# Kernel tuning notes

Measured on AMD Instinct MI355X. Metric: run time of the kernel, lower is better.

Reference implementation:

```python
import jax, jax.numpy as jnp
import numpy as np

N_NODES = 50000
N_EDGES = 800000
N_IN = 96
N_HID = 96
N_CLS = 16
P_DROP = 0.5


def setup_inputs() -> dict:
    key = jax.random.key(0)
    ks = jax.random.split(key, 10)
    return {
        "features": jax.random.normal(ks[0], (N_NODES, N_IN), dtype=jnp.float32),
        "edge_weight": jax.random.uniform(ks[1], (N_EDGES,), dtype=jnp.float32),
        "src": jax.random.randint(ks[2], (N_EDGES,), 0, N_NODES),
        "dst": jax.random.randint(ks[3], (N_EDGES,), 0, N_NODES),
        "W0": jax.random.normal(ks[4], (N_IN, N_HID), dtype=jnp.float32) / np.sqrt(N_IN).astype(np.float32),
        "b0": jnp.zeros((N_HID,), dtype=jnp.float32),
        "W1": jax.random.normal(ks[5], (N_HID, N_HID), dtype=jnp.float32) / np.sqrt(N_HID).astype(np.float32),
        "b1": jnp.zeros((N_HID,), dtype=jnp.float32),
        "W2": jax.random.normal(ks[6], (N_HID, N_CLS), dtype=jnp.float32) / np.sqrt(N_HID).astype(np.float32),
        "b2": jnp.zeros((N_CLS,), dtype=jnp.float32),
    }


def reference(features, edge_weight, src, dst, W0, b0, W1, b1, W2, b2):
    N = features.shape[0]
    # Unweighted node degrees (DGL GraphConv norm='both'), clamped to >= 1.
    ones_e = jnp.ones_like(edge_weight)
    out_deg = jnp.clip(jax.ops.segment_sum(ones_e, src, num_segments=N), 1.0)
    in_deg = jnp.clip(jax.ops.segment_sum(ones_e, dst, num_segments=N), 1.0)
    inv_sqrt_out = out_deg ** -0.5  # [N]
    inv_sqrt_in = in_deg ** -0.5    # [N]

    def graph_conv(h, W, b, act):
        h = h * inv_sqrt_out[:, None]
        m = h[src] * edge_weight[:, None]                   # [E, d] gather + edge scale
        agg = jax.ops.segment_sum(m, dst, num_segments=N)   # [N, d] scatter-add
        out = (agg * inv_sqrt_in[:, None]) @ W + b          # D_in^-1/2, then linear + bias
        return act(out) if act is not None else out

    layers = [(W0, b0, jax.nn.relu), (W1, b1, jax.nn.relu), (W2, b2, None)]
    dkey = jax.random.key(42)
    h = features
    for i, (W, b, act) in enumerate(layers):
        keep = jax.random.bernoulli(jax.random.fold_in(dkey, i), 1.0 - P_DROP, h.shape)
        h = jnp.where(keep, h / (1.0 - P_DROP), 0.0)        # dropout p=0.5
        h = graph_conv(h, W, b, act)
    return jax.nn.log_softmax(h, axis=1)
```

## Files before the change

kernel.cpp:

```cpp
#include <hip/hip_runtime.h>
#include <hip/hip_fp16.h>
#include <stdint.h>

#define NNODES 50000
#define NEDGES 800000
#define NHID 96
#define NCLS 16

#define NC 100
#define NR 4
#define EPB (NEDGES / NC)
#define RNODES (NNODES / NR)
#define RWORDS8 (RNODES / 4)
#define NWORDS8 (NNODES / 4)
#define SCANB ((NWORDS8 + 255) / 256)
#define HISTBLKS (NC * NR)
#define FEPT 4
#define FILLB2 ((NEDGES / FEPT + 255) / 256)
#define NDROP4 ((NNODES * NHID / 4 + 255) / 256)

__host__ __device__ inline void tf2x32(uint32_t k0, uint32_t k1, uint32_t x0, uint32_t x1,
                                       uint32_t& o0, uint32_t& o1) {
  uint32_t k2 = k0 ^ k1 ^ 0x1BD11BDAu;
#define TFROT(v, r) (((v) << (r)) | ((v) >> (32 - (r))))
#define TFR(r) { x0 += x1; x1 = TFROT(x1, r); x1 ^= x0; }
  x0 += k0; x1 += k1;
  TFR(13) TFR(15) TFR(26) TFR(6)
  x0 += k1; x1 += k2 + 1u;
  TFR(17) TFR(29) TFR(16) TFR(24)
  x0 += k2; x1 += k0 + 2u;
  TFR(13) TFR(15) TFR(26) TFR(6)
  x0 += k0; x1 += k1 + 3u;
  TFR(17) TFR(29) TFR(16) TFR(24)
  x0 += k1; x1 += k2 + 4u;
  TFR(13) TFR(15) TFR(26) TFR(6)
  x0 += k2; x1 += k0 + 5u;
  o0 = x0; o1 = x1;
#undef TFR
#undef TFROT
}

__device__ inline bool keep_bit(uint32_t k0, uint32_t k1, uint32_t j) {
  uint32_t o0, o1;
  tf2x32(k0, k1, 0u, j, o0, o1);
  return (((o0 ^ o1) >> 31) == 0u);
}

__global__ __launch_bounds__(256) void hist_drop_kernel(
    const int* __restrict__ src, const int* __restrict__ dst,
    uint32_t* __restrict__ slabD, uint32_t* __restrict__ slabS,
    uint8_t* __restrict__ rank8, uint32_t* __restrict__ flags,
    const float* __restrict__ h, float* __restrict__ X,
    uint32_t k0, uint32_t k1) {
  __shared__ uint32_t HD[RWORDS8];
  __shared__ uint32_t HS[RWORDS8];
  const int tid = threadIdx.x, b = blockIdx.x;
  if (b >= HISTBLKS) {
    int j = ((b - HISTBLKS) * 256 + tid) * 4;
    if (j < NNODES * NHID) {
      float4 hv = *(const float4*)(h + j);
      float4 o;
      o.x = keep_bit(k0, k1, (uint32_t)(j + 0)) ? hv.x * 2.0f : 0.0f;
      o.y = keep_bit(k0, k1, (uint32_t)(j + 1)) ? hv.y * 2.0f : 0.0f;
      o.z = keep_bit(k0, k1, (uint32_t)(j + 2)) ? hv.z * 2.0f : 0.0f;
      o.w = keep_bit(k0, k1, (uint32_t)(j + 3)) ? hv.w * 2.0f : 0.0f;
      *(float4*)(X + j) = o;
    }
    return;
  }
  if (b == 0 && tid < SCANB) flags[tid] = 0;
  const int c = b / NR, r = b - c * NR;
  const int e0 = c * EPB, e1 = e0 + EPB;
  const int nbase = r * RNODES;
  for (int w = tid; w < RWORDS8; w += 256) { HD[w] = 0; HS[w] = 0; }
  __syncthreads();
  int e = e0 + tid;
  for (; e + 768 < e1; e += 1024) {
    int d0 = dst[e] - nbase,       d1 = dst[e + 256] - nbase;
    int d2 = dst[e + 512] - nbase, d3 = dst[e + 768] - nbase;
    int s0 = src[e] - nbase,       s1 = src[e + 256] - nbase;
    int s2 = src[e + 512] - nbase, s3 = src[e + 768] - nbase;
    if ((unsigned)d0 < (unsigned)RNODES) {
      int sh = (d0 & 3) * 8;
      uint32_t old = atomicAdd(&HD[d0 >> 2], 1u << sh);
      rank8[e] = (uint8_t)((old >> sh) & 0xFFu);
    }
    if ((unsigned)d1 < (unsigned)RNODES) {
      int sh = (d1 & 3) * 8;
      uint32_t old = atomicAdd(&HD[d1 >> 2], 1u << sh);
      rank8[e + 256] = (uint8_t)((old >> sh) & 0xFFu);
    }
    if ((unsigned)d2 < (unsigned)RNODES) {
      int sh = (d2 & 3) * 8;
      uint32_t old = atomicAdd(&HD[d2 >> 2], 1u << sh);
      rank8[e + 512] = (uint8_t)((old >> sh) & 0xFFu);
    }
    if ((unsigned)d3 < (unsigned)RNODES) {
      int sh = (d3 & 3) * 8;
      uint32_t old = atomicAdd(&HD[d3 >> 2], 1u << sh);
      rank8[e + 768] = (uint8_t)((old >> sh) & 0xFFu);
    }
    if ((unsigned)s0 < (unsigned)RNODES) atomicAdd(&HS[s0 >> 2], 1u << ((s0 & 3) * 8));
    if ((unsigned)s1 < (unsigned)RNODES) atomicAdd(&HS[s1 >> 2], 1u << ((s1 & 3) * 8));
    if ((unsigned)s2 < (unsigned)RNODES) atomicAdd(&HS[s2 >> 2], 1u << ((s2 & 3) * 8));
    if ((unsigned)s3 < (unsigned)RNODES) atomicAdd(&HS[s3 >> 2], 1u << ((s3 & 3) * 8));
  }
  for (; e < e1; e += 256) {
    int d = dst[e] - nbase;
    if ((unsigned)d < (unsigned)RNODES) {
      int sh = (d & 3) * 8;
      uint32_t old = atomicAdd(&HD[d >> 2], 1u << sh);
      rank8[e] = (uint8_t)((old >> sh) & 0xFFu);
    }
    int s = src[e] - nbase;
    if ((unsigned)s < (unsigned)RNODES) atomicAdd(&HS[s >> 2], 1u << ((s & 3) * 8));
  }
  __syncthreads();
  uint32_t* dpD = slabD + (size_t)b * RWORDS8;
  uint32_t* dpS = slabS + (size_t)b * RWORDS8;
  for (int w = tid; w < RWORDS8; w += 256) { dpD[w] = HD[w]; dpS[w] = HS[w]; }
}

__global__ __launch_bounds__(256) void reduce_scan_kernel(
    const uint32_t* __restrict__ slabD, const uint32_t* __restrict__ slabS,
    float* __restrict__ inv_o, float* __restrict__ inv_i,
    uint32_t* __restrict__ rel8, int* __restrict__ row_ptr,
    uint32_t* __restrict__ flags) {
  __shared__ int lds[256];
  __shared__ int base_s;
  const int tid = threadIdx.x, b = blockIdx.x;
  const int gw = b * 256 + tid;
  uint32_t runD = 0, runS = 0;
  int n0 = 0;
  if (gw < NWORDS8) {
    int r = gw / RWORDS8, lw = gw - r * RWORDS8;
    n0 = r * RNODES + 4 * lw;
#pragma unroll 4
    for (int c = 0; c < NC; ++c) {
      rel8[(size_t)c * NWORDS8 + gw] = runD;
      runD += slabD[(size_t)(c * NR + r) * RWORDS8 + lw];
      runS += slabS[(size_t)(c * NR + r) * RWORDS8 + lw];
    }
  }
  const int d0 = runD & 0xFF, d1 = (runD >> 8) & 0xFF,
            d2 = (runD >> 16) & 0xFF, d3 = runD >> 24;
  const int tsum = d0 + d1 + d2 + d3;
  lds[tid] = tsum;
  __syncthreads();
  for (int off = 1; off < 256; off <<= 1) {
    int t = (tid >= off) ? lds[tid - off] : 0;
    __syncthreads();
    lds[tid] += t;
    __syncthreads();
  }
  const int incl = lds[tid];
  if (tid == 255) atomicExch(&flags[b], 0x80000000u | (uint32_t)lds[255]);
  if (tid < 64) {
    uint32_t part = 0;
    if (tid < b) {
      uint32_t v;
      do { v = atomicAdd(&flags[tid], 0u); } while (!(v & 0x80000000u));
      part = v & 0x7FFFFFFFu;
    }
#pragma unroll
    for (int off = 32; off > 0; off >>= 1)
      part += __shfl_down((unsigned)part, off, 64);
    if (tid == 0) base_s = (int)part;
  }
  __syncthreads();
  const int base = base_s;
  if (gw < NWORDS8) {
    int excl = base + incl - tsum;
    *(int4*)(row_ptr + n0) = make_int4(excl, excl + d0, excl + d0 + d1, excl + d0 + d1 + d2);
    *(float4*)(inv_i + n0) = make_float4(
        rsqrtf(fmaxf((float)d0, 1.0f)), rsqrtf(fmaxf((float)d1, 1.0f)),
        rsqrtf(fmaxf((float)d2, 1.0f)), rsqrtf(fmaxf((float)d3, 1.0f)));
    int o0 = runS & 0xFF, o1 = (runS >> 8) & 0xFF, o2 = (runS >> 16) & 0xFF, o3 = runS >> 24;
    *(float4*)(inv_o + n0) = make_float4(
        rsqrtf(fmaxf((float)o0, 1.0f)), rsqrtf(fmaxf((float)o1, 1.0f)),
        rsqrtf(fmaxf((float)o2, 1.0f)), rsqrtf(fmaxf((float)o3, 1.0f)));
    if (gw == NWORDS8 - 1) row_ptr[NNODES] = NEDGES;
  }
}

__global__ __launch_bounds__(256) void fill_kernel(
    const int* __restrict__ src, const int* __restrict__ dst, const float* __restrict__ ew,
    const uint8_t* __restrict__ rank8, const uint32_t* __restrict__ rel8,
    const int* __restrict__ row_ptr, const float* __restrict__ inv_o,
    uint32_t* __restrict__ csr) {
  int t = blockIdx.x * 256 + threadIdx.x;
  int e = t * 4;
  if (e >= NEDGES) return;
  int4 d4 = *(const int4*)(dst + e);
  int4 s4 = *(const int4*)(src + e);
  float4 w4 = *(const float4*)(ew + e);
  uint32_t r4 = *(const uint32_t*)(rank8 + e);
  const uint32_t* rel = rel8 + (size_t)(e / EPB) * NWORDS8;
#pragma unroll
  for (int k = 0; k < 4; ++k) {
    int d = (&d4.x)[k];
    int s = (&s4.x)[k];
    float w = (&w4.x)[k] * inv_o[s];
    int rk = (int)((r4 >> (k * 8)) & 0xFFu);
    int sh = (d & 3) * 8;
    int rel_v = (int)((rel[d >> 2] >> sh) & 0xFFu);
    int pos = row_ptr[d] + rel_v + rk;
    uint32_t v = ((uint32_t)s << 16) | (uint32_t)__half_as_ushort(__float2half_rn(w));
    if ((unsigned)pos < (unsigned)NEDGES) csr[pos] = v;
  }
}

__global__ __launch_bounds__(256) void gemm96_kernel(
    const float* __restrict__ X, const float* __restrict__ W, __half* __restrict__ Yh) {
  __shared__ float Wl[96 * 96];
  const int tid = threadIdx.x;
  {
    const float4* Wg = (const float4*)W;
    float4* Ws = (float4*)Wl;
#pragma unroll
    for (int i = 0; i < 9; ++i)
      Ws[tid + i * 256] = Wg[tid + i * 256];
  }
  __syncthreads();

  const int cg = tid & 7;
  const int rq = tid >> 3;
  const int row0 = blockIdx.x * 128 + rq * 4;
  const int c0 = cg * 12;

  float acc[4][12];
#pragma unroll
  for (int r = 0; r < 4; ++r)
#pragma unroll
    for (int c = 0; c < 12; ++c) acc[r][c] = 0.f;

  const float* xr[4];
#pragma unroll
  for (int r = 0; r < 4; ++r) {
    int rr = row0 + r; if (rr > NNODES - 1) rr = NNODES - 1;
    xr[r] = X + (size_t)rr * 96;
  }

  for (int k = 0; k < 96; k += 4) {
    float4 x4[4];
#pragma unroll
    for (int r = 0; r < 4; ++r) x4[r] = *(const float4*)(xr[r] + k);
#pragma unroll
    for (int kk = 0; kk < 4; ++kk) {
      const float4* wp = (const float4*)(Wl + (k + kk) * 96 + c0);
      float4 w0 = wp[0], w1 = wp[1], w2 = wp[2];
      float xv[4] = { (&x4[0].x)[kk], (&x4[1].x)[kk], (&x4[2].x)[kk], (&x4[3].x)[kk] };
#pragma unroll
      for (int r = 0; r < 4; ++r) {
        acc[r][0]  += xv[r] * w0.x; acc[r][1]  += xv[r] * w0.y;
        acc[r][2]  += xv[r] * w0.z; acc[r][3]  += xv[r] * w0.w;
        acc[r][4]  += xv[r] * w1.x; acc[r][5]  += xv[r] * w1.y;
        acc[r][6]  += xv[r] * w1.z; acc[r][7]  += xv[r] * w1.w;
        acc[r][8]  += xv[r] * w2.x; acc[r][9]  += xv[r] * w2.y;
        acc[r][10] += xv[r] * w2.z; acc[r][11] += xv[r] * w2.w;
      }
    }
  }

#pragma unroll
  for (int r = 0; r < 4; ++r) {
    int rr = row0 + r;
    if (rr < NNODES) {
      __half2* hp = (__half2*)(Yh + (size_t)rr * 96 + c0);
#pragma unroll
      for (int c = 0; c < 6; ++c)
        hp[c] = __floats2half2_rn(acc[r][2 * c], acc[r][2 * c + 1]);
    }
  }
}

__global__ __launch_bounds__(256) void gemm16_kernel(
    const float* __restrict__ X, const float* __restrict__ W, __half* __restrict__ Y2h) {
  __shared__ float Wl[96 * 16];
  const int tid = threadIdx.x;
  {
    const float4* Wg = (const float4*)W;
    float4* Ws = (float4*)Wl;
    for (int i = tid; i < 384; i += 256) Ws[i] = Wg[i];
  }
  __syncthreads();

  const int row0 = blockIdx.x * 512 + tid * 2;
  const float* xr[2];
#pragma unroll
  for (int r = 0; r < 2; ++r) {
    int rr = row0 + r; if (rr > NNODES - 1) rr = NNODES - 1;
    xr[r] = X + (size_t)rr * 96;
  }

  float acc[2][16];
#pragma unroll
  for (int r = 0; r < 2; ++r)
#pragma unroll
    for (int c = 0; c < 16; ++c) acc[r][c] = 0.f;

  for (int k = 0; k < 96; k += 4) {
    float4 x4[2];
#pragma unroll
    for (int r = 0; r < 2; ++r) x4[r] = *(const float4*)(xr[r] + k);
#pragma unroll
    for (int kk = 0; kk < 4; ++kk) {
      const float4* wp = (const float4*)(Wl + (k + kk) * 16);
      float4 w0 = wp[0], w1 = wp[1], w2 = wp[2], w3 = wp[3];
#pragma unroll
      for (int r = 0; r < 2; ++r) {
        float xv = (&x4[r].x)[kk];
        acc[r][0]  += xv * w0.x; acc[r][1]  += xv * w0.y;
        acc[r][2]  += xv * w0.z; acc[r][3]  += xv * w0.w;
        acc[r][4]  += xv * w1.x; acc[r][5]  += xv * w1.y;
        acc[r][6]  += xv * w1.z; acc[r][7]  += xv * w1.w;
        acc[r][8]  += xv * w2.x; acc[r][9]  += xv * w2.y;
        acc[r][10] += xv * w2.z; acc[r][11] += xv * w2.w;
        acc[r][12] += xv * w3.x; acc[r][13] += xv * w3.y;
        acc[r][14] += xv * w3.z; acc[r][15] += xv * w3.w;
      }
    }
  }

#pragma unroll
  for (int r = 0; r < 2; ++r) {
    int rr = row0 + r;
    if (rr < NNODES) {
      __half2* hp = (__half2*)(Y2h + (size_t)rr * 16);
#pragma unroll
      for (int c = 0; c < 8; ++c)
        hp[c] = __floats2half2_rn(acc[r][2 * c], acc[r][2 * c + 1]);
    }
  }
}

#define ACC8(u0, wt) { \
  float2 g0 = __half22float2(*(__half2*)&u0.x); \
  float2 g1 = __half22float2(*(__half2*)&u0.y); \
  float2 g2 = __half22float2(*(__half2*)&u0.z); \
  float2 g3 = __half22float2(*(__half2*)&u0.w); \
  acc[0] += g0.x * wt; acc[1] += g0.y * wt; \
  acc[2] += g1.x * wt; acc[3] += g1.y * wt; \
  acc[4] += g2.x * wt; acc[5] += g2.y * wt; \
  acc[6] += g3.x * wt; acc[7] += g3.y * wt; }

__global__ __launch_bounds__(256) void gather96_drop_kernel(
    const __half* __restrict__ Yh, const uint32_t* __restrict__ csr,
    const int* __restrict__ row_ptr, const float* __restrict__ inv_in,
    const float* __restrict__ bias,
    float* __restrict__ Xn, uint32_t k0, uint32_t k1) {
  int tid = blockIdx.x * 256 + threadIdx.x;
  int n = tid / 12;
  int q = tid - n * 12;
  if (n >= NNODES) return;
  int beg = row_ptr[n], end = row_ptr[n + 1];
  float acc[8];
#pragma unroll
  for (int i = 0; i < 8; ++i) acc[i] = 0.f;

  int p = beg;
  for (; p + 8 <= end; p += 8) {
    uint32_t pw[8];
#pragma unroll
    for (int i = 0; i < 8; ++i) pw[i] = csr[p + i];
    float wv[8];
    uint4 u[8];
#pragma unroll
    for (int i = 0; i < 8; ++i) {
      int s = (int)(pw[i] >> 16); if (s >= NNODES) s = 0;
      wv[i] = __half2float(__ushort_as_half((unsigned short)(pw[i] & 0xFFFFu)));
      u[i] = *(const uint4*)(Yh + (size_t)s * 96 + q * 8);
    }
#pragma unroll
    for (int i = 0; i < 8; ++i) { ACC8(u[i], wv[i]) }
  }
  for (; p + 2 <= end; p += 2) {
    uint32_t pa = csr[p], pb = csr[p + 1];
    int s0 = pa >> 16, s1 = pb >> 16;
    if (s0 >= NNODES) s0 = 0;
    if (s1 >= NNODES) s1 = 0;
    float w0 = __half2float(__ushort_as_half((unsigned short)(pa & 0xFFFFu)));
    float w1 = __half2float(__ushort_as_half((unsigned short)(pb & 0xFFFFu)));
    uint4 a0 = *(const uint4*)(Yh + (size_t)s0 * 96 + q * 8);
    uint4 b0 = *(const uint4*)(Yh + (size_t)s1 * 96 + q * 8);
    ACC8(a0, w0)
    ACC8(b0, w1)
  }
  if (p < end) {
    uint32_t pa = csr[p];
    int s0 = pa >> 16;
    if (s0 >= NNODES) s0 = 0;
    float w0 = __half2float(__ushort_as_half((unsigned short)(pa & 0xFFFFu)));
    uint4 a0 = *(const uint4*)(Yh + (size_t)s0 * 96 + q * 8);
    ACC8(a0, w0)
  }

  float iv = inv_in[n];
  const float* bp = bias + q * 8;
  float o[8];
#pragma unroll
  for (int i = 0; i < 8; ++i)
    o[i] = fmaxf(acc[i] * iv + bp[i], 0.f) * 2.0f;
  uint32_t jb = (uint32_t)(n * 96 + q * 8);
#pragma unroll
  for (int i = 0; i < 8; ++i)
    o[i] = keep_bit(k0, k1, jb + i) ? o[i] : 0.f;
  float* xp = Xn + (size_t)n * 96 + q * 8;
  *(float4*)(xp + 0) = make_float4(o[0], o[1], o[2], o[3]);
  *(float4*)(xp + 4) = make_float4(o[4], o[5], o[6], o[7]);
}

__global__ __launch_bounds__(256) void gather16_lsm_kernel(
    const __half* __restrict__ Y2h, const uint32_t* __restrict__ csr,
    const int* __restrict__ row_ptr, const float* __restrict__ inv_in,
    const float* __restrict__ b2, float* __restrict__ out) {
  int t = blockIdx.x * 256 + threadIdx.x;
  int n = t >> 1;
  int q = t & 1;
  if (n >= NNODES) return;
  int beg = row_ptr[n], end = row_ptr[n + 1];
  float acc[8];
#pragma unroll
  for (int i = 0; i < 8; ++i) acc[i] = 0.f;

  int p = beg;
  for (; p + 4 <= end; p += 4) {
    uint32_t pa = csr[p], pb = csr[p + 1], pc = csr[p + 2], pd = csr[p + 3];
    int sa = pa >> 16, sb = pb >> 16, sc_ = pc >> 16, sd = pd >> 16;
    if (sa >= NNODES) sa = 0;
    if (sb >= NNODES) sb = 0;
    if (sc_ >= NNODES) sc_ = 0;
    if (sd >= NNODES) sd = 0;
    float wa = __half2float(__ushort_as_half((unsigned short)(pa & 0xFFFFu)));
    float wb = __half2float(__ushort_as_half((unsigned short)(pb & 0xFFFFu)));
    float wc = __half2float(__ushort_as_half((unsigned short)(pc & 0xFFFFu)));
    float wd = __half2float(__ushort_as_half((unsigned short)(pd & 0xFFFFu)));
    uint4 a0 = *(const uint4*)(Y2h + (size_t)sa * 16 + q * 8);
    uint4 b0 = *(const uint4*)(Y2h + (size_t)sb * 16 + q * 8);
    uint4 c0 = *(const uint4*)(Y2h + (size_t)sc_ * 16 + q * 8);
    uint4 d0 = *(const uint4*)(Y2h + (size_t)sd * 16 + q * 8);
    ACC8(a0, wa) ACC8(b0, wb) ACC8(c0, wc) ACC8(d0, wd)
  }
  for (; p + 2 <= end; p += 2) {
    uint32_t pa = csr[p], pb = csr[p + 1];
    int sa = pa >> 16, sb = pb >> 16;
    if (sa >= NNODES) sa = 0;
    if (sb >= NNODES) sb = 0;
    float wa = __half2float(__ushort_as_half((unsigned short)(pa & 0xFFFFu)));
    float wb = __half2float(__ushort_as_half((unsigned short)(pb & 0xFFFFu)));
    uint4 a0 = *(const uint4*)(Y2h + (size_t)sa * 16 + q * 8);
    uint4 b0 = *(const uint4*)(Y2h + (size_t)sb * 16 + q * 8);
    ACC8(a0, wa) ACC8(b0, wb)
  }
  if (p < end) {
    uint32_t pa = csr[p];
    int sa = pa >> 16;
    if (sa >= NNODES) sa = 0;
    float wa = __half2float(__ushort_as_half((unsigned short)(pa & 0xFFFFu)));
    uint4 a0 = *(const uint4*)(Y2h + (size_t)sa * 16 + q * 8);
    ACC8(a0, wa)
  }

  float iv = inv_in[n];
  float v[8];
#pragma unroll
  for (int i = 0; i < 8; ++i) v[i] = acc[i] * iv + b2[q * 8 + i];
  float m = v[0];
#pragma unroll
  for (int i = 1; i < 8; i++) m = fmaxf(m, v[i]);
  m = fmaxf(m, __shfl_xor(m, 1));
  float s = 0.f;
#pragma unroll
  for (int i = 0; i < 8; i++) s += expf(v[i] - m);
  s += __shfl_xor(s, 1);
  float ls = logf(s);
  float* orow = out + (size_t)n * 16 + q * 8;
  *(float4*)(orow + 0) = make_float4(v[0] - m - ls, v[1] - m - ls, v[2] - m - ls, v[3] - m - ls);
  *(float4*)(orow + 4) = make_float4(v[4] - m - ls, v[5] - m - ls, v[6] - m - ls, v[7] - m - ls);
}

extern "C" void kernel_launch(void* const* d_in, const int* in_sizes, int n_in,
                              void* d_out, int out_size, void* d_ws, size_t ws_size,
                              hipStream_t stream) {
  const float* feat = (const float*)d_in[0];
  const float* ew   = (const float*)d_in[1];
  const int*   src  = (const int*)d_in[2];
  const int*   dst  = (const int*)d_in[3];
  const float* W0   = (const float*)d_in[4];
  const float* b0   = (const float*)d_in[5];
  const float* W1   = (const float*)d_in[6];
  const float* b1   = (const float*)d_in[7];
  const float* W2   = (const float*)d_in[8];
  const float* b2   = (const float*)d_in[9];
  float* out = (float*)d_out;

  char* base = (char*)d_ws;
  size_t off = 0;
  auto take = [&](size_t nbytes) {
    void* q = base + off;
    off += (nbytes + 255) & ~(size_t)255;
    return q;
  };
  uint32_t* flags   = (uint32_t*)take((size_t)SCANB * 4);
  int*      row_ptr = (int*)take((size_t)(NNODES + 1) * 4);
  float*    inv_o   = (float*)take((size_t)NNODES * 4);
  float*    inv_i   = (float*)take((size_t)NNODES * 4);
  uint32_t* slabD   = (uint32_t*)take((size_t)NC * NR * RWORDS8 * 4);
  uint32_t* slabS   = (uint32_t*)take((size_t)NC * NR * RWORDS8 * 4);
  uint32_t* rel8    = (uint32_t*)take((size_t)NC * NWORDS8 * 4);
  uint8_t*  rank8   = (uint8_t*)take((size_t)NEDGES);
  uint32_t* csr     = (uint32_t*)take((size_t)NEDGES * 4);
  float*    X       = (float*)take((size_t)NNODES * NHID * 4);
  __half*   Yh      = (__half*)take((size_t)NNODES * NHID * 2);
  __half*   Y2h     = (__half*)take((size_t)NNODES * NCLS * 2);
  (void)ws_size; (void)in_sizes; (void)n_in; (void)out_size;

  uint32_t k[3][2];
  for (uint32_t i = 0; i < 3; i++) tf2x32(0u, 42u, 0u, i, k[i][0], k[i][1]);

  hist_drop_kernel<<<HISTBLKS + NDROP4, 256, 0, stream>>>(
      src, dst, slabD, slabS, rank8, flags, feat, X, k[0][0], k[0][1]);
  reduce_scan_kernel<<<SCANB, 256, 0, stream>>>(slabD, slabS, inv_o, inv_i, rel8, row_ptr, flags);
  fill_kernel<<<FILLB2, 256, 0, stream>>>(src, dst, ew, rank8, rel8, row_ptr, inv_o, csr);

  const int G96  = (NNODES + 127) / 128;
  const int G16  = (NNODES + 511) / 512;
  const int GGD  = (NNODES * 12 + 255) / 256;
  const int GLSM = (NNODES * 2 + 255) / 256;

  gemm96_kernel<<<G96, 256, 0, stream>>>(X, W0, Yh);
  gather96_drop_kernel<<<GGD, 256, 0, stream>>>(Yh, csr, row_ptr, inv_i, b0, X, k[1][0], k[1][1]);
  gemm96_kernel<<<G96, 256, 0, stream>>>(X, W1, Yh);
  gather96_drop_kernel<<<GGD, 256, 0, stream>>>(Yh, csr, row_ptr, inv_i, b1, X, k[2][0], k[2][1]);
  gemm16_kernel<<<G16, 256, 0, stream>>>(X, W2, Y2h);
  gather16_lsm_kernel<<<GLSM, 256, 0, stream>>>(Y2h, csr, row_ptr, inv_i, b2, out);
}
```

Baseline: 265.5 us.

## Fuse scan, CSR fill and first GEMM into one kernel launch

Merges the reduce/scan, CSR fill and layer-0 GEMM into a single launch. Scan blocks signal completion through a global counter, and fill blocks spin-wait on it. GEMM blocks are independent of both, so they run alongside. Fill now handles 8 edges per thread instead of 4. This removes two launch boundaries and lets the GEMM overlap the scan and fill. The cost is spin-wait blocks holding CUs, and a deadlock risk if fill blocks are scheduled before the scan blocks finish.

Result: slower. 288.9 us (+8.8%).

```diff
diff --git a/kernel.cpp b/kernel.cpp
--- a/kernel.cpp
+++ b/kernel.cpp
@@ -15,9 +15,11 @@
 #define NWORDS8 (NNODES / 4)
 #define SCANB ((NWORDS8 + 255) / 256)
 #define HISTBLKS (NC * NR)
-#define FEPT 4
-#define FILLB2 ((NEDGES / FEPT + 255) / 256)
 #define NDROP4 ((NNODES * NHID / 4 + 255) / 256)
+#define FEPT8 8
+#define FILLB3 ((NEDGES / FEPT8 + 255) / 256)
+#define G96B ((NNODES + 127) / 128)
+#define DONE_IDX 64
 
 __host__ __device__ inline void tf2x32(uint32_t k0, uint32_t k1, uint32_t x0, uint32_t x1,
                                        uint32_t& o0, uint32_t& o1) {
@@ -68,7 +70,7 @@
     }
     return;
   }
-  if (b == 0 && tid < SCANB) flags[tid] = 0;
+  if (b == 0 && tid < 128) flags[tid] = 0;
   const int c = b / NR, r = b - c * NR;
   const int e0 = c * EPB, e1 = e0 + EPB;
   const int nbase = r * RNODES;
@@ -121,92 +123,167 @@
   for (int w = tid; w < RWORDS8; w += 256) { dpD[w] = HD[w]; dpS[w] = HS[w]; }
 }
 
-__global__ __launch_bounds__(256) void reduce_scan_kernel(
+__global__ __launch_bounds__(256) void scan_fill_gemm_kernel(
     const uint32_t* __restrict__ slabD, const uint32_t* __restrict__ slabS,
     float* __restrict__ inv_o, float* __restrict__ inv_i,
     uint32_t* __restrict__ rel8, int* __restrict__ row_ptr,
-    uint32_t* __restrict__ flags) {
-  __shared__ int lds[256];
-  __shared__ int base_s;
+    uint32_t* __restrict__ flags,
+    const int* __restrict__ src, const int* __restrict__ dst,
+    const float* __restrict__ ew, const uint8_t* __restrict__ rank8,
+    uint32_t* __restrict__ csr,
+    const float* __restrict__ X, const float* __restrict__ W, __half* __restrict__ Yh) {
+  __shared__ float Wl[96 * 96];
   const int tid = threadIdx.x, b = blockIdx.x;
-  const int gw = b * 256 + tid;
-  uint32_t runD = 0, runS = 0;
-  int n0 = 0;
-  if (gw < NWORDS8) {
-    int r = gw / RWORDS8, lw = gw - r * RWORDS8;
-    n0 = r * RNODES + 4 * lw;
+
+  if (b < SCANB) {
+    int* lds = (int*)Wl;
+    __shared__ int base_s;
+    const int gw = b * 256 + tid;
+    uint32_t runD = 0, runS = 0;
+    int n0 = 0;
+    if (gw < NWORDS8) {
+      int r = gw / RWORDS8, lw = gw - r * RWORDS8;
+      n0 = r * RNODES + 4 * lw;
 #pragma unroll 4
-    for (int c = 0; c < NC; ++c) {
-      rel8[(size_t)c * NWORDS8 + gw] = runD;
-      runD += slabD[(size_t)(c * NR + r) * RWORDS8 + lw];
-      runS += slabS[(size_t)(c * NR + r) * RWORDS8 + lw];
-    }
-  }
-  const int d0 = runD & 0xFF, d1 = (runD >> 8) & 0xFF,
-            d2 = (runD >> 16) & 0xFF, d3 = runD >> 24;
-  const int tsum = d0 + d1 + d2 + d3;
-  lds[tid] = tsum;
+      for (int c = 0; c < NC; ++c) {
+        rel8[(size_t)c * NWORDS8 + gw] = runD;
+        runD += slabD[(size_t)(c * NR + r) * RWORDS8 + lw];
+        runS += slabS[(size_t)(c * NR + r) * RWORDS8 + lw];
+      }
+    }
+    const int d0 = runD & 0xFF, d1 = (runD >> 8) & 0xFF,
+              d2 = (runD >> 16) & 0xFF, d3 = runD >> 24;
+    const int tsum = d0 + d1 + d2 + d3;
+    lds[tid] = tsum;
+    __syncthreads();
+    for (int off = 1; off < 256; off <<= 1) {
+      int t = (tid >= off) ? lds[tid - off] : 0;
+      __syncthreads();
+      lds[tid] += t;
+      __syncthreads();
+    }
+    const int incl = lds[tid];
+    if (tid == 255) atomicExch(&flags[b], 0x80000000u | (uint32_t)lds[255]);
+    if (tid < 64) {
+      uint32_t part = 0;
+      if (tid < b) {
+        uint32_t v;
+        do { v = atomicAdd(&flags[tid], 0u); } while (!(v & 0x80000000u));
+        part = v & 0x7FFFFFFFu;
+      }
+#pragma unroll
+      for (int off = 32; off > 0; off >>= 1)
+        part += __shfl_down((unsigned)part, off, 64);
+      if (tid == 0) base_s = (int)part;
+    }
+    __syncthreads();
+    const int base = base_s;
+    if (gw < NWORDS8) {
+      int excl = base + incl - tsum;
+      *(int4*)(row_ptr + n0) = make_int4(excl, excl + d0, excl + d0 + d1, excl + d0 + d1 + d2);
+      *(float4*)(inv_i + n0) = make_float4(
+          rsqrtf(fmaxf((float)d0, 1.0f)), rsqrtf(fmaxf((float)d1, 1.0f)),
+          rsqrtf(fmaxf((float)d2, 1.0f)), rsqrtf(fmaxf((float)d3, 1.0f)));
+      int o0 = runS & 0xFF, o1 = (runS >> 8) & 0xFF, o2 = (runS >> 16) & 0xFF, o3 = runS >> 24;
+      *(float4*)(inv_o + n0) = make_float4(
+          rsqrtf(fmaxf((float)o0, 1.0f)), rsqrtf(fmaxf((float)o1, 1.0f)),
+          rsqrtf(fmaxf((float)o2, 1.0f)), rsqrtf(fmaxf((float)o3, 1.0f)));
+      if (gw == NWORDS8 - 1) row_ptr[NNODES] = NEDGES;
+    }
+    __threadfence();
+    __syncthreads();
+    if (tid == 0) atomicAdd(&flags[DONE_IDX], 1u);
+    return;
+  }
+
+  if (b < SCANB + FILLB3) {
+    if (tid == 0) {
+      while (atomicAdd(&flags[DONE_IDX], 0u) < (uint32_t)SCANB)
+        __builtin_amdgcn_s_sleep(8);
+    }
+    __syncthreads();
+    __threadfence();
+    int t = (b - SCANB) * 256 + tid;
+    int e = t * 8;
+    if (e >= NEDGES) return;
+    const uint32_t* rel = rel8 + (size_t)(e / EPB) * NWORDS8;
+    int4 dA = *(const int4*)(dst + e), dB = *(const int4*)(dst + e + 4);
+    int4 sA = *(const int4*)(src + e), sB = *(const int4*)(src + e + 4);
+    float4 wA = *(const float4*)(ew + e), wB = *(const float4*)(ew + e + 4);
+    uint2 r8 = *(const uint2*)(rank8 + e);
+#pragma unroll
+    for (int k = 0; k < 8; ++k) {
+      int d = (k < 4) ? (&dA.x)[k] : (&dB.x)[k - 4];
+      int s = (k < 4) ? (&sA.x)[k] : (&sB.x)[k - 4];
+      float w = ((k < 4) ? (&wA.x)[k] : (&wB.x)[k - 4]) * inv_o[s];
+      int rk = (int)(((k < 4 ? r8.x : r8.y) >> ((k & 3) * 8)) & 0xFFu);
+      int sh = (d & 3) * 8;
+      int rel_v = (int)((rel[d >> 2] >> sh) & 0xFFu);
+      int pos = row_ptr[d] + rel_v + rk;
+      uint32_t v = ((uint32_t)s << 16) | (uint32_t)__half_as_ushort(__float2half_rn(w));
+      if ((unsigned)pos < (unsigned)NEDGES) csr[pos] = v;
+    }
+    return;
+  }
+
+  const int gb = b - SCANB - FILLB3;
+  {
+    const float4* Wg = (const float4*)W;
+    float4* Ws = (float4*)Wl;
+#pragma unroll
+    for (int i = 0; i < 9; ++i)
+      Ws[tid + i * 256] = Wg[tid + i * 256];
+  }
   __syncthreads();
-  for (int off = 1; off < 256; off <<= 1) {
-    int t = (tid >= off) ? lds[tid - off] : 0;
-    __syncthreads();
-    lds[tid] += t;
-    __syncthreads();
-  }
-  const int incl = lds[tid];
-  if (tid == 255) atomicExch(&flags[b], 0x80000000u | (uint32_t)lds[255]);
-  if (tid < 64) {
-    uint32_t part = 0;
-    if (tid < b) {
-      uint32_t v;
-      do { v = atomicAdd(&flags[tid], 0u); } while (!(v & 0x80000000u));
-      part = v & 0x7FFFFFFFu;
-    }
-#pragma unroll
-    for (int off = 32; off > 0; off >>= 1)
-      part += __shfl_down((unsigned)part, off, 64);
-    if (tid == 0) base_s = (int)part;
-  }
-  __syncthreads();
-  const int base = base_s;
-  if (gw < NWORDS8) {
-    int excl = base + incl - tsum;
-    *(int4*)(row_ptr + n0) = make_int4(excl, excl + d0, excl + d0 + d1, excl + d0 + d1 + d2);
-    *(float4*)(inv_i + n0) = make_float4(
-        rsqrtf(fmaxf((float)d0, 1.0f)), rsqrtf(fmaxf((float)d1, 1.0f)),
-        rsqrtf(fmaxf((float)d2, 1.0f)), rsqrtf(fmaxf((float)d3, 1.0f)));
-    int o0 = runS & 0xFF, o1 = (runS >> 8) & 0xFF, o2 = (runS >> 16) & 0xFF, o3 = runS >> 24;
-    *(float4*)(inv_o + n0) = make_float4(
-        rsqrtf(fmaxf((float)o0, 1.0f)), rsqrtf(fmaxf((float)o1, 1.0f)),
-        rsqrtf(fmaxf((float)o2, 1.0f)), rsqrtf(fmaxf((float)o3, 1.0f)));
-    if (gw == NWORDS8 - 1) row_ptr[NNODES] = NEDGES;
-  }
-}
-
-__global__ __launch_bounds__(256) void fill_kernel(
-    const int* __restrict__ src, const int* __restrict__ dst, const float* __restrict__ ew,
-    const uint8_t* __restrict__ rank8, const uint32_t* __restrict__ rel8,
-    const int* __restrict__ row_ptr, const float* __restrict__ inv_o,
-    uint32_t* __restrict__ csr) {
-  int t = blockIdx.x * 256 + threadIdx.x;
-  int e = t * 4;
-  if (e >= NEDGES) return;
-  int4 d4 = *(const int4*)(dst + e);
-  int4 s4 = *(const int4*)(src + e);
-  float4 w4 = *(const float4*)(ew + e);
-  uint32_t r4 = *(const uint32_t*)(rank8 + e);
-  const uint32_t* rel = rel8 + (size_t)(e / EPB) * NWORDS8;
-#pragma unroll
-  for (int k = 0; k < 4; ++k) {
-    int d = (&d4.x)[k];
-    int s = (&s4.x)[k];
-    float w = (&w4.x)[k] * inv_o[s];
-    int rk = (int)((r4 >> (k * 8)) & 0xFFu);
-    int sh = (d & 3) * 8;
-    int rel_v = (int)((rel[d >> 2] >> sh) & 0xFFu);
-    int pos = row_ptr[d] + rel_v + rk;
-    uint32_t v = ((uint32_t)s << 16) | (uint32_t)__half_as_ushort(__float2half_rn(w));
-    if ((unsigned)pos < (unsigned)NEDGES) csr[pos] = v;
+
+  const int cg = tid & 7;
+  const int rq = tid >> 3;
+  const int row0 = gb * 128 + rq * 4;
+  const int c0 = cg * 12;
+
+  float acc[4][12];
+#pragma unroll
+  for (int r = 0; r < 4; ++r)
+#pragma unroll
+    for (int c = 0; c < 12; ++c) acc[r][c] = 0.f;
+
+  const float* xr[4];
+#pragma unroll
+  for (int r = 0; r < 4; ++r) {
+    int rr = row0 + r; if (rr > NNODES - 1) rr = NNODES - 1;
+    xr[r] = X + (size_t)rr * 96;
+  }
+
+  for (int k = 0; k < 96; k += 4) {
+    float4 x4[4];
+#pragma unroll
+    for (int r = 0; r < 4; ++r) x4[r] = *(const float4*)(xr[r] + k);
+#pragma unroll
+    for (int kk = 0; kk < 4; ++kk) {
+      const float4* wp = (const float4*)(Wl + (k + kk) * 96 + c0);
+      float4 w0 = wp[0], w1 = wp[1], w2 = wp[2];
+      float xv[4] = { (&x4[0].x)[kk], (&x4[1].x)[kk], (&x4[2].x)[kk], (&x4[3].x)[kk] };
+#pragma unroll
+      for (int r = 0; r < 4; ++r) {
+        acc[r][0]  += xv[r] * w0.x; acc[r][1]  += xv[r] * w0.y;
+        acc[r][2]  += xv[r] * w0.z; acc[r][3]  += xv[r] * w0.w;
+        acc[r][4]  += xv[r] * w1.x; acc[r][5]  += xv[r] * w1.y;
+        acc[r][6]  += xv[r] * w1.z; acc[r][7]  += xv[r] * w1.w;
+        acc[r][8]  += xv[r] * w2.x; acc[r][9]  += xv[r] * w2.y;
+        acc[r][10] += xv[r] * w2.z; acc[r][11] += xv[r] * w2.w;
+      }
+    }
+  }
+
+#pragma unroll
+  for (int r = 0; r < 4; ++r) {
+    int rr = row0 + r;
+    if (rr < NNODES) {
+      __half2* hp = (__half2*)(Yh + (size_t)rr * 96 + c0);
+#pragma unroll
+      for (int c = 0; c < 6; ++c)
+        hp[c] = __floats2half2_rn(acc[r][2 * c], acc[r][2 * c + 1]);
+    }
   }
 }
 
@@ -501,7 +578,7 @@
     off += (nbytes + 255) & ~(size_t)255;
     return q;
   };
-  uint32_t* flags   = (uint32_t*)take((size_t)SCANB * 4);
+  uint32_t* flags   = (uint32_t*)take((size_t)128 * 4);
   int*      row_ptr = (int*)take((size_t)(NNODES + 1) * 4);
   float*    inv_o   = (float*)take((size_t)NNODES * 4);
   float*    inv_i   = (float*)take((size_t)NNODES * 4);
@@ -520,17 +597,16 @@
 
   hist_drop_kernel<<<HISTBLKS + NDROP4, 256, 0, stream>>>(
       src, dst, slabD, slabS, rank8, flags, feat, X, k[0][0], k[0][1]);
-  reduce_scan_kernel<<<SCANB, 256, 0, stream>>>(slabD, slabS, inv_o, inv_i, rel8, row_ptr, flags);
-  fill_kernel<<<FILLB2, 256, 0, stream>>>(src, dst, ew, rank8, rel8, row_ptr, inv_o, csr);
-
-  const int G96  = (NNODES + 127) / 128;
+  scan_fill_gemm_kernel<<<SCANB + FILLB3 + G96B, 256, 0, stream>>>(
+      slabD, slabS, inv_o, inv_i, rel8, row_ptr, flags,
+      src, dst, ew, rank8, csr, X, W0, Yh);
+
   const int G16  = (NNODES + 511) / 512;
   const int GGD  = (NNODES * 12 + 255) / 256;
   const int GLSM = (NNODES * 2 + 255) / 256;
 
-  gemm96_kernel<<<G96, 256, 0, stream>>>(X, W0, Yh);
   gather96_drop_kernel<<<GGD, 256, 0, stream>>>(Yh, csr, row_ptr, inv_i, b0, X, k[1][0], k[1][1]);
-  gemm96_kernel<<<G96, 256, 0, stream>>>(X, W1, Yh);
+  gemm96_kernel<<<G96B, 256, 0, stream>>>(X, W1, Yh);
   gather96_drop_kernel<<<GGD, 256, 0, stream>>>(Yh, csr, row_ptr, inv_i, b1, X, k[2][0], k[2][1]);
   gemm16_kernel<<<G16, 256, 0, stream>>>(X, W2, Y2h);
   gather16_lsm_kernel<<<GLSM, 256, 0, stream>>>(Y2h, csr, row_ptr, inv_i, b2, out);
```
